# Kernel optimization log

Measured on AMD Instinct MI355X. Metric: run time of the kernel, lower is better.

Reference implementation:

```python
import jax, jax.numpy as jnp
import numpy as np
import math

HAD = 1024  # hadamard_size hard-coded in HiggsLinear

def _hadamard_matrix(n):
    H = np.array([[1.0]], dtype=np.float32)
    while H.shape[0] < n:
        H = np.block([[H, H], [H, -H]])
    return H

# normalized Hadamard (scale = 1/sqrt(1024)); symmetric, so x @ _H == H x per block
_H = jnp.asarray(_hadamard_matrix(HAD) / math.sqrt(HAD))

def setup_inputs() -> dict:
    key = jax.random.key(0)
    k1, k2, k3, k4, k5 = jax.random.split(key, 5)
    in_f, out_f, d, n_codes, tokens = 4096, 4096, 2, 256, 8192
    return {
        "x": jax.random.normal(k1, (tokens, in_f), jnp.float32),
        "codes": jax.random.randint(k2, (out_f, in_f // d), 0, n_codes, jnp.int32),
        "grid": jax.random.normal(k3, (n_codes, d), jnp.float32),
        "scales": jax.random.uniform(k4, (out_f, in_f // HAD), jnp.float32, 0.5, 1.5),
        "bias": jax.random.normal(k5, (out_f,), jnp.float32),
    }

def reference(x, codes, grid, scales, bias):
    d = grid.shape[1]
    out_f = codes.shape[0]
    post = ((HAD - 1) // d + 1) * d  # post_hadamard_size
    # --- dequantize weight: codebook gather + per-hadamard-group scale ---
    W = grid[codes]                               # (out, num_higgs_groups, d)
    W = W.reshape(out_f, -1, post)[..., :HAD]     # (out, n_had_groups, 1024)
    W = W * scales[..., None]
    W = W.reshape(out_f, -1)                      # (out, in)
    # --- blockwise Hadamard transform of input (block = 1024) ---
    nh = x.shape[-1] // HAD
    xh = x.reshape(x.shape[:-1] + (nh, HAD)) @ _H
    xh = xh.reshape(x.shape[:-1] + (nh * HAD,))
    # --- fused dequant matmul equivalent: F.linear(xh, W, bias) ---
    return xh @ W.T + bias
```

## Files before the change

### kernel.cpp

```cpp
#include <hip/hip_runtime.h>

#define M_TOK 8192
#define N_OUT 4096
#define K_IN  4096
#define NT    (K_IN / 64)
#define CVT_BLOCKS ((M_TOK * K_IN) / 2048)
#define DEQ_BLOCKS (N_OUT * 4 / 4)

typedef __bf16 bf16x8 __attribute__((ext_vector_type(8)));
typedef float f32x4 __attribute__((ext_vector_type(4)));

__device__ __forceinline__ unsigned short f2b(float f) {
  union { float f; unsigned u; } c; c.f = f;
  unsigned u = c.u;
  return (unsigned short)((u + 0x7FFFu + ((u >> 16) & 1u)) >> 16);
}

__global__ __launch_bounds__(256) void prep_kernel(const float* __restrict__ x,
                                                   unsigned short* __restrict__ xb,
                                                   const int* __restrict__ codes,
                                                   const float* __restrict__ grid,
                                                   const float* __restrict__ scales,
                                                   unsigned short* __restrict__ Wt) {
  if (blockIdx.x < CVT_BLOCKS) {
    long i = ((long)blockIdx.x * 256 + threadIdx.x) * 8;
    float4 a = *(const float4*)(x + i);
    float4 b = *(const float4*)(x + i + 4);
    union { unsigned short us[8]; uint4 v; } o;
    o.us[0] = f2b(a.x); o.us[1] = f2b(a.y); o.us[2] = f2b(a.z); o.us[3] = f2b(a.w);
    o.us[4] = f2b(b.x); o.us[5] = f2b(b.y); o.us[6] = f2b(b.z); o.us[7] = f2b(b.w);
    *(uint4*)(xb + i) = o.v;
  } else {
    int bid = blockIdx.x - CVT_BLOCKS;
    int wave = threadIdx.x >> 6;
    int lane = threadIdx.x & 63;
    int G = bid * 4 + wave;
    int o = G >> 2;
    int g = G & 3;
    const int* crow = codes + (long)o * 2048 + g * 512 + lane * 8;
    int4 c0 = *(const int4*)crow;
    int4 c1 = *(const int4*)(crow + 4);
    float v[16];
    const float2* g2p = (const float2*)grid;
    float2 t;
    t = g2p[c0.x]; v[0] = t.x;  v[1] = t.y;
    t = g2p[c0.y]; v[2] = t.x;  v[3] = t.y;
    t = g2p[c0.z]; v[4] = t.x;  v[5] = t.y;
    t = g2p[c0.w]; v[6] = t.x;  v[7] = t.y;
    t = g2p[c1.x]; v[8] = t.x;  v[9] = t.y;
    t = g2p[c1.y]; v[10] = t.x; v[11] = t.y;
    t = g2p[c1.z]; v[12] = t.x; v[13] = t.y;
    t = g2p[c1.w]; v[14] = t.x; v[15] = t.y;
#pragma unroll
    for (int s = 1; s < 16; s <<= 1) {
#pragma unroll
      for (int base = 0; base < 16; base++) {
        if (!(base & s)) {
          float a = v[base], b = v[base | s];
          v[base] = a + b;
          v[base | s] = a - b;
        }
      }
    }
#pragma unroll
    for (int m = 1; m <= 32; m <<= 1) {
      bool hi = (lane & m) != 0;
#pragma unroll
      for (int c = 0; c < 16; c++) {
        float p = __shfl_xor(v[c], m, 64);
        v[c] = hi ? p - v[c] : p + v[c];
      }
    }
    float sc = scales[o * 4 + g] * 0.03125f;
    union { unsigned short us[16]; uint4 q[2]; } out;
#pragma unroll
    for (int c = 0; c < 16; c++) out.us[c] = f2b(v[c] * sc);
    unsigned short* wp = Wt + (long)o * 4096 + g * 1024 + lane * 16;
    *(uint4*)wp = out.q[0];
    *(uint4*)(wp + 8) = out.q[1];
  }
}

__device__ __forceinline__ void load16_to_lds(const unsigned short* g, unsigned short* l) {
  __builtin_amdgcn_global_load_lds((const __attribute__((address_space(1))) void*)g,
                                   (__attribute__((address_space(3))) void*)l,
                                   16, 0, 0);
}

__device__ __forceinline__ void phase_barrier() {
  __builtin_amdgcn_s_barrier();
  __builtin_amdgcn_sched_barrier(0);
}

__global__ __launch_bounds__(512, 2) void gemm_kernel(const unsigned short* __restrict__ A,
                                                      const unsigned short* __restrict__ B,
                                                      const float* __restrict__ bias,
                                                      float* __restrict__ C) {
  __shared__ unsigned short sA[2][256 * 64];
  __shared__ unsigned short sB[2][256 * 64];

  const int wg  = blockIdx.x;
  const int swz = (wg & 7) * (512 / 8) + (wg >> 3);
  const int bn  = (swz & 15) * 256;
  const int bm  = (swz >> 4) * 256;

  const int tid  = threadIdx.x;
  const int wave = tid >> 6;
  const int lane = tid & 63;
  const int wm   = wave >> 2;
  const int wn   = wave & 3;

  const long K = K_IN;
  const unsigned short* aSrc[4];
  const unsigned short* bSrc[4];
  unsigned short* aDst[4];
  unsigned short* bDst[4];
#pragma unroll
  for (int j = 0; j < 4; j++) {
    const int g   = tid + j * 512;
    const int row = g >> 3;
    const int cg  = (g & 7) ^ (row & 7);
    aSrc[j] = A + (long)(bm + row) * K + cg * 8;
    bSrc[j] = B + (long)(bn + row) * K + cg * 8;
    aDst[j] = &sA[0][g * 8];
    bDst[j] = &sB[0][g * 8];
  }

  const int m7  = lane & 7;
  const int cb  = lane >> 4;
  const int r0a = wm * 128 + (lane & 15);
  const int r0b = wn * 64  + (lane & 15);
  const int aoff0 = (r0a * 8 + ( cb      ^ m7)) * 8;
  const int aoff1 = (r0a * 8 + ((cb | 4) ^ m7)) * 8;
  const int boff0 = (r0b * 8 + ( cb      ^ m7)) * 8;
  const int boff1 = (r0b * 8 + ((cb | 4) ^ m7)) * 8;

  f32x4 acc[8][4] = {};

  load16_to_lds(bSrc[0], bDst[0]);
  load16_to_lds(bSrc[1], bDst[1]);
  load16_to_lds(bSrc[2], bDst[2]);
  load16_to_lds(bSrc[3], bDst[3]);
  load16_to_lds(aSrc[0], aDst[0]);
  load16_to_lds(aSrc[2], aDst[2]);
  load16_to_lds(aSrc[1], aDst[1]);
  load16_to_lds(aSrc[3], aDst[3]);
  asm volatile("s_waitcnt vmcnt(2)" ::: "memory");
  phase_barrier();

  for (int t = 0; t < NT; t++) {
    const int p = t & 1;
    const unsigned short* bufA = &sA[p][0];
    const unsigned short* bufB = &sB[p][0];
    const bool pf   = (t + 1 < NT);
    const int  koff = (t + 1) * 64;
    const int  q16  = (p ^ 1) * 16384;

    bf16x8 a0[4], a1[4], b0[4];

#pragma unroll
    for (int i = 0; i < 4; i++) b0[i] = *(const bf16x8*)(bufB + boff0 + i * 1024);
#pragma unroll
    for (int i = 0; i < 4; i++) a0[i] = *(const bf16x8*)(bufA + aoff0 + i * 1024);
    if (pf) {
      load16_to_lds(bSrc[0] + koff, bDst[0] + q16);
      load16_to_lds(bSrc[1] + koff, bDst[1] + q16);
    }
    phase_barrier();
    __builtin_amdgcn_s_setprio(1);
#pragma unroll
    for (int mi = 0; mi < 4; mi++)
#pragma unroll
      for (int ni = 0; ni < 4; ni++)
        acc[mi][ni] = __builtin_amdgcn_mfma_f32_16x16x32_bf16(a0[mi], b0[ni], acc[mi][ni], 0, 0, 0);
    __builtin_amdgcn_s_setprio(0);
    if (pf) asm volatile("s_waitcnt vmcnt(2)" ::: "memory");
    else    asm volatile("s_waitcnt vmcnt(0)" ::: "memory");
    phase_barrier();

#pragma unroll
    for (int i = 0; i < 4; i++) a1[i] = *(const bf16x8*)(bufA + aoff0 + 4096 + i * 1024);
    if (pf) {
      load16_to_lds(bSrc[2] + koff, bDst[2] + q16);
      load16_to_lds(bSrc[3] + koff, bDst[3] + q16);
    }
    phase_barrier();
    __builtin_amdgcn_s_setprio(1);
#pragma unroll
    for (int mi = 0; mi < 4; mi++)
#pragma unroll
      for (int ni = 0; ni < 4; ni++)
        acc[4 + mi][ni] = __builtin_amdgcn_mfma_f32_16x16x32_bf16(a1[mi], b0[ni], acc[4 + mi][ni], 0, 0, 0);
    __builtin_amdgcn_s_setprio(0);
    phase_barrier();

#pragma unroll
    for (int i = 0; i < 4; i++) b0[i] = *(const bf16x8*)(bufB + boff1 + i * 1024);
#pragma unroll
    for (int i = 0; i < 4; i++) a0[i] = *(const bf16x8*)(bufA + aoff1 + i * 1024);
    if (pf) {
      load16_to_lds(aSrc[0] + koff, aDst[0] + q16);
      load16_to_lds(aSrc[2] + koff, aDst[2] + q16);
    }
    phase_barrier();
    __builtin_amdgcn_s_setprio(1);
#pragma unroll
    for (int mi = 0; mi < 4; mi++)
#pragma unroll
      for (int ni = 0; ni < 4; ni++)
        acc[mi][ni] = __builtin_amdgcn_mfma_f32_16x16x32_bf16(a0[mi], b0[ni], acc[mi][ni], 0, 0, 0);
    __builtin_amdgcn_s_setprio(0);
    phase_barrier();

#pragma unroll
    for (int i = 0; i < 4; i++) a1[i] = *(const bf16x8*)(bufA + aoff1 + 4096 + i * 1024);
    if (pf) {
      load16_to_lds(aSrc[1] + koff, aDst[1] + q16);
      load16_to_lds(aSrc[3] + koff, aDst[3] + q16);
    }
    phase_barrier();
    __builtin_amdgcn_s_setprio(1);
#pragma unroll
    for (int mi = 0; mi < 4; mi++)
#pragma unroll
      for (int ni = 0; ni < 4; ni++)
        acc[4 + mi][ni] = __builtin_amdgcn_mfma_f32_16x16x32_bf16(a1[mi], b0[ni], acc[4 + mi][ni], 0, 0, 0);
    __builtin_amdgcn_s_setprio(0);
    if (pf) asm volatile("s_waitcnt vmcnt(2)" ::: "memory");
    phase_barrier();
  }

  const int cn  = lane & 15;
  const int cm4 = (lane >> 4) * 4;
#pragma unroll
  for (int ni = 0; ni < 4; ni++) {
    const int col = bn + wn * 64 + ni * 16 + cn;
    const float bb = bias[col];
#pragma unroll
    for (int mi = 0; mi < 8; mi++) {
#pragma unroll
      for (int r = 0; r < 4; r++) {
        const int row = bm + wm * 128 + mi * 16 + cm4 + r;
        C[(long)row * N_OUT + col] = acc[mi][ni][r] + bb;
      }
    }
  }
}

extern "C" void kernel_launch(void* const* d_in, const int* in_sizes, int n_in,
                              void* d_out, int out_size, void* d_ws, size_t ws_size,
                              hipStream_t stream) {
  const float* x      = (const float*)d_in[0];
  const int*   codes  = (const int*)d_in[1];
  const float* grid   = (const float*)d_in[2];
  const float* scales = (const float*)d_in[3];
  const float* bias   = (const float*)d_in[4];
  float* out = (float*)d_out;

  unsigned short* xb = (unsigned short*)d_ws;
  unsigned short* Wt = xb + (size_t)M_TOK * K_IN;

  prep_kernel<<<CVT_BLOCKS + DEQ_BLOCKS, 256, 0, stream>>>(x, xb, codes, grid, scales, Wt);
  gemm_kernel<<<512, 512, 0, stream>>>(xb, Wt, bias, out);
}
```

Before: 546.6 us.

## Deepen GEMM global-to-LDS prefetch to two tiles ahead and reorder MFMA phases

The main bf16 GEMM loop now issues global-to-LDS loads for tile t+2 into the buffer being consumed, where it previously loaded tile t+1 into the other buffer. It also reorders the four MFMA phases so that B fragments for both k-halves stay in registers (bk0/bk1) while A fragments are reloaded. Both changes aim to hide global memory latency behind more compute. The cost is more in-flight loads, more B registers, and fragile vmcnt bookkeeping with a risk of overwriting LDS data that is still being read.

```diff
diff --git a/kernel.cpp b/kernel.cpp
--- a/kernel.cpp
+++ b/kernel.cpp
@@ -145,88 +145,96 @@
   load16_to_lds(aSrc[2], aDst[2]);
   load16_to_lds(aSrc[1], aDst[1]);
   load16_to_lds(aSrc[3], aDst[3]);
-  asm volatile("s_waitcnt vmcnt(2)" ::: "memory");
+  load16_to_lds(bSrc[0] + 64, bDst[0] + 16384);
+  load16_to_lds(bSrc[1] + 64, bDst[1] + 16384);
+  load16_to_lds(bSrc[2] + 64, bDst[2] + 16384);
+  load16_to_lds(bSrc[3] + 64, bDst[3] + 16384);
+  load16_to_lds(aSrc[0] + 64, aDst[0] + 16384);
+  load16_to_lds(aSrc[2] + 64, aDst[2] + 16384);
+  load16_to_lds(aSrc[1] + 64, aDst[1] + 16384);
+  load16_to_lds(aSrc[3] + 64, aDst[3] + 16384);
+  asm volatile("s_waitcnt vmcnt(10)" ::: "memory");
   phase_barrier();
 
   for (int t = 0; t < NT; t++) {
     const int p = t & 1;
     const unsigned short* bufA = &sA[p][0];
     const unsigned short* bufB = &sB[p][0];
-    const bool pf   = (t + 1 < NT);
-    const int  koff = (t + 1) * 64;
-    const int  q16  = (p ^ 1) * 16384;
-
-    bf16x8 a0[4], a1[4], b0[4];
-
-#pragma unroll
-    for (int i = 0; i < 4; i++) b0[i] = *(const bf16x8*)(bufB + boff0 + i * 1024);
-#pragma unroll
-    for (int i = 0; i < 4; i++) a0[i] = *(const bf16x8*)(bufA + aoff0 + i * 1024);
+    const bool pf   = (t + 2 < NT);
+    const int  koff = (t + 2) * 64;
+    const int  q16  = p * 16384;
+
+    bf16x8 av[4], bk0[4], bk1[4];
+
+#pragma unroll
+    for (int i = 0; i < 4; i++) bk0[i] = *(const bf16x8*)(bufB + boff0 + i * 1024);
+#pragma unroll
+    for (int i = 0; i < 4; i++) av[i]  = *(const bf16x8*)(bufA + aoff0 + i * 1024);
+    phase_barrier();
+    __builtin_amdgcn_s_setprio(1);
+#pragma unroll
+    for (int mi = 0; mi < 4; mi++)
+#pragma unroll
+      for (int ni = 0; ni < 4; ni++)
+        acc[mi][ni] = __builtin_amdgcn_mfma_f32_16x16x32_bf16(av[mi], bk0[ni], acc[mi][ni], 0, 0, 0);
+    __builtin_amdgcn_s_setprio(0);
+    phase_barrier();
+
+#pragma unroll
+    for (int i = 0; i < 4; i++) bk1[i] = *(const bf16x8*)(bufB + boff1 + i * 1024);
+#pragma unroll
+    for (int i = 0; i < 4; i++) av[i]  = *(const bf16x8*)(bufA + aoff1 + i * 1024);
+    phase_barrier();
     if (pf) {
       load16_to_lds(bSrc[0] + koff, bDst[0] + q16);
       load16_to_lds(bSrc[1] + koff, bDst[1] + q16);
     }
-    phase_barrier();
-    __builtin_amdgcn_s_setprio(1);
-#pragma unroll
-    for (int mi = 0; mi < 4; mi++)
-#pragma unroll
-      for (int ni = 0; ni < 4; ni++)
-        acc[mi][ni] = __builtin_amdgcn_mfma_f32_16x16x32_bf16(a0[mi], b0[ni], acc[mi][ni], 0, 0, 0);
-    __builtin_amdgcn_s_setprio(0);
-    if (pf) asm volatile("s_waitcnt vmcnt(2)" ::: "memory");
-    else    asm volatile("s_waitcnt vmcnt(0)" ::: "memory");
-    phase_barrier();
-
-#pragma unroll
-    for (int i = 0; i < 4; i++) a1[i] = *(const bf16x8*)(bufA + aoff0 + 4096 + i * 1024);
+    __builtin_amdgcn_s_setprio(1);
+#pragma unroll
+    for (int mi = 0; mi < 4; mi++)
+#pragma unroll
+      for (int ni = 0; ni < 4; ni++)
+        acc[mi][ni] = __builtin_amdgcn_mfma_f32_16x16x32_bf16(av[mi], bk1[ni], acc[mi][ni], 0, 0, 0);
+    __builtin_amdgcn_s_setprio(0);
+    if (t < NT - 2)      asm volatile("s_waitcnt vmcnt(10)" ::: "memory");
+    else if (t == NT - 2) asm volatile("s_waitcnt vmcnt(8)" ::: "memory");
+    else                 asm volatile("s_waitcnt vmcnt(0)" ::: "memory");
+    phase_barrier();
+
+#pragma unroll
+    for (int i = 0; i < 4; i++) av[i] = *(const bf16x8*)(bufA + aoff0 + 4096 + i * 1024);
+    phase_barrier();
     if (pf) {
       load16_to_lds(bSrc[2] + koff, bDst[2] + q16);
       load16_to_lds(bSrc[3] + koff, bDst[3] + q16);
-    }
-    phase_barrier();
-    __builtin_amdgcn_s_setprio(1);
-#pragma unroll
-    for (int mi = 0; mi < 4; mi++)
-#pragma unroll
-      for (int ni = 0; ni < 4; ni++)
-        acc[4 + mi][ni] = __builtin_amdgcn_mfma_f32_16x16x32_bf16(a1[mi], b0[ni], acc[4 + mi][ni], 0, 0, 0);
-    __builtin_amdgcn_s_setprio(0);
-    phase_barrier();
-
-#pragma unroll
-    for (int i = 0; i < 4; i++) b0[i] = *(const bf16x8*)(bufB + boff1 + i * 1024);
-#pragma unroll
-    for (int i = 0; i < 4; i++) a0[i] = *(const bf16x8*)(bufA + aoff1 + i * 1024);
-    if (pf) {
       load16_to_lds(aSrc[0] + koff, aDst[0] + q16);
       load16_to_lds(aSrc[2] + koff, aDst[2] + q16);
     }
-    phase_barrier();
-    __builtin_amdgcn_s_setprio(1);
-#pragma unroll
-    for (int mi = 0; mi < 4; mi++)
-#pragma unroll
-      for (int ni = 0; ni < 4; ni++)
-        acc[mi][ni] = __builtin_amdgcn_mfma_f32_16x16x32_bf16(a0[mi], b0[ni], acc[mi][ni], 0, 0, 0);
-    __builtin_amdgcn_s_setprio(0);
-    phase_barrier();
-
-#pragma unroll
-    for (int i = 0; i < 4; i++) a1[i] = *(const bf16x8*)(bufA + aoff1 + 4096 + i * 1024);
+    __builtin_amdgcn_s_setprio(1);
+#pragma unroll
+    for (int mi = 0; mi < 4; mi++)
+#pragma unroll
+      for (int ni = 0; ni < 4; ni++)
+        acc[4 + mi][ni] = __builtin_amdgcn_mfma_f32_16x16x32_bf16(av[mi], bk0[ni], acc[4 + mi][ni], 0, 0, 0);
+    __builtin_amdgcn_s_setprio(0);
+    phase_barrier();
+
+#pragma unroll
+    for (int i = 0; i < 4; i++) av[i] = *(const bf16x8*)(bufA + aoff1 + 4096 + i * 1024);
+    phase_barrier();
     if (pf) {
       load16_to_lds(aSrc[1] + koff, aDst[1] + q16);
       load16_to_lds(aSrc[3] + koff, aDst[3] + q16);
     }
-    phase_barrier();
-    __builtin_amdgcn_s_setprio(1);
-#pragma unroll
-    for (int mi = 0; mi < 4; mi++)
-#pragma unroll
-      for (int ni = 0; ni < 4; ni++)
-        acc[4 + mi][ni] = __builtin_amdgcn_mfma_f32_16x16x32_bf16(a1[mi], b0[ni], acc[4 + mi][ni], 0, 0, 0);
-    __builtin_amdgcn_s_setprio(0);
-    if (pf) asm volatile("s_waitcnt vmcnt(2)" ::: "memory");
+    __builtin_amdgcn_s_setprio(1);
+#pragma unroll
+    for (int mi = 0; mi < 4; mi++)
+#pragma unroll
+      for (int ni = 0; ni < 4; ni++)
+        acc[4 + mi][ni] = __builtin_amdgcn_mfma_f32_16x16x32_bf16(av[mi], bk1[ni], acc[4 + mi][ni], 0, 0, 0);
+    __builtin_amdgcn_s_setprio(0);
+    if (t < NT - 2)      asm volatile("s_waitcnt vmcnt(10)" ::: "memory");
+    else if (t == NT - 2) asm volatile("s_waitcnt vmcnt(2)" ::: "memory");
     phase_barrier();
   }
 
```

New measurement: 553.8 us. About the same (+1.3%).
